# Performance work log

Hardware: AMD Instinct MI355X
Metric: run time of the kernel (lower is better)

Reference implementation:

```python
import jax, jax.numpy as jnp
import numpy as np

B, S, E, H = 4, 2048, 1024, 16
DK = E // H

def setup_inputs() -> dict:
    key = jax.random.key(0)
    ks = jax.random.split(key, 5)
    scale = 1.0 / np.sqrt(E)
    return {
        "x":  jax.random.normal(ks[0], (B, S, E), dtype=jnp.float32),
        "Wq": jax.random.normal(ks[1], (E, E), dtype=jnp.float32) * scale,
        "Wk": jax.random.normal(ks[2], (E, E), dtype=jnp.float32) * scale,
        "Wv": jax.random.normal(ks[3], (E, E), dtype=jnp.float32) * scale,
        "Wo": jax.random.normal(ks[4], (E, E), dtype=jnp.float32) * scale,
    }

def reference(x, Wq, Wk, Wv, Wo):
    b, s, e = x.shape
    # nn.Linear (no bias): y = x @ W.T
    def split_heads(t):  # (b, s, e) -> (b, H, s, DK)
        return t.reshape(b, s, H, DK).transpose(0, 2, 1, 3)
    Q = split_heads(x @ Wq.T)
    K = split_heads(x @ Wk.T)
    V = split_heads(x @ Wv.T)
    scores = jnp.einsum('bhqd,bhkd->bhqk', Q, K) / jnp.sqrt(jnp.float32(DK))
    attn = jax.nn.softmax(scores, axis=-1)  # dropout p=0.0 -> identity
    ctx = jnp.einsum('bhqk,bhkd->bhqd', attn, V)
    concat = ctx.transpose(0, 2, 1, 3).reshape(b, s, e)
    return concat @ Wo.T
```

## Files before the change

kernel.cpp:

```cpp
#include <hip/hip_runtime.h>


typedef __bf16 bf16x8 __attribute__((ext_vector_type(8)));
typedef __bf16 bf16x4 __attribute__((ext_vector_type(4)));
typedef float floatx4 __attribute__((ext_vector_type(4)));
typedef unsigned int uint2v __attribute__((ext_vector_type(2)));

#define GLOAD_LDS16(gp, lp) __builtin_amdgcn_global_load_lds( \
    (const __attribute__((address_space(1))) unsigned int*)(gp), \
    (__attribute__((address_space(3))) unsigned int*)(lp), 16, 0, 0)

__global__ __launch_bounds__(256) void cvt_x(const float4* __restrict__ s,
                                             bf16x4* __restrict__ d, int n4) {
    int i = blockIdx.x * 256 + threadIdx.x;
    if (i < n4) {
        float4 v = s[i];
        bf16x4 o = { (__bf16)v.x, (__bf16)v.y, (__bf16)v.z, (__bf16)v.w };
        d[i] = o;
    }
}

__global__ __launch_bounds__(256) void cvt_w(const float4* __restrict__ Wq,
                                             const float4* __restrict__ Wk,
                                             const float4* __restrict__ Wv,
                                             const float4* __restrict__ Wo,
                                             bf16x4* __restrict__ oq, bf16x4* __restrict__ ok,
                                             bf16x4* __restrict__ ov, bf16x4* __restrict__ oo,
                                             float qscale) {
    int y = blockIdx.y;
    const float4* s = (y == 0) ? Wq : (y == 1) ? Wk : (y == 2) ? Wv : Wo;
    bf16x4* d = (y == 0) ? oq : (y == 1) ? ok : (y == 2) ? ov : oo;
    float scale = (y == 0) ? qscale : 1.0f;
    int i = blockIdx.x * 256 + threadIdx.x;
    float4 v = s[i];
    bf16x4 o = { (__bf16)(v.x * scale), (__bf16)(v.y * scale),
                 (__bf16)(v.z * scale), (__bf16)(v.w * scale) };
    d[i] = o;
}


__device__ __forceinline__ void gemm_stage(const __bf16* __restrict__ A,
                                           const __bf16* __restrict__ W,
                                           __bf16* Asm, __bf16* Bsm,
                                           int bm, int bn, int k0, int w, int lane) {
#pragma unroll
    for (int j = 0; j < 2; ++j) {
        int base = j * 256 + w * 64;
        int flat = base + lane;
        int c = flat >> 7, r = flat & 127;
        GLOAD_LDS16(A + (size_t)(bm + r) * 1024 + k0 + c * 8, (char*)Asm + base * 16);
    }
#pragma unroll
    for (int j = 0; j < 4; ++j) {
        int base = j * 256 + w * 64;
        int flat = base + lane;
        int c = flat >> 8, r = flat & 255;
        GLOAD_LDS16(W + (size_t)(bn + r) * 1024 + k0 + c * 8, (char*)Bsm + base * 16);
    }
}

__device__ __forceinline__ void gemm_phase(const __bf16* __restrict__ A,
                                           const __bf16* __restrict__ W,
                                           const __bf16* Asm_r, const __bf16* Bsm_r,
                                           __bf16* Asm_s, __bf16* Bsm_s,
                                           int bm, int bn, int ks,
                                           int w, int lane, int quad, int l15,
                                           int wy, int wx,
                                           floatx4 acc[4][8]) {
    gemm_stage(A, W, Asm_s, Bsm_s, bm, bn, ks, w, lane);
    __builtin_amdgcn_sched_barrier(0);
    asm volatile("s_waitcnt vmcnt(12)" ::: "memory");
    __builtin_amdgcn_s_barrier();
    __builtin_amdgcn_sched_barrier(0);

    bf16x8 af[4], bf[8];
#pragma unroll
    for (int mt = 0; mt < 4; ++mt)
        af[mt] = *(const bf16x8*)(Asm_r + (quad * 128 + wy * 64 + mt * 16 + l15) * 8);
#pragma unroll
    for (int nt = 0; nt < 8; ++nt)
        bf[nt] = *(const bf16x8*)(Bsm_r + (quad * 256 + wx * 128 + nt * 16 + l15) * 8);
#pragma unroll
    for (int mt = 0; mt < 4; ++mt)
#pragma unroll
        for (int nt = 0; nt < 8; ++nt)
            acc[mt][nt] = __builtin_amdgcn_mfma_f32_16x16x32_bf16(af[mt], bf[nt],
                                                                  acc[mt][nt], 0, 0, 0);
    __builtin_amdgcn_sched_barrier(0);
    __builtin_amdgcn_s_barrier();
}

__device__ __forceinline__ void gemm_mainloop3(const __bf16* __restrict__ A,
                                               const __bf16* __restrict__ W,
                                               __bf16* SM,
                                               int bm, int bn, int tid,
                                               floatx4 acc[4][8]) {
    const int w = tid >> 6, lane = tid & 63;
    const int quad = lane >> 4, l15 = lane & 15;
    const int wy = w >> 1, wx = w & 1;
    __bf16* As[3] = { SM, SM + 12288, SM + 24576 };
    __bf16* Bs[3] = { SM + 4096, SM + 16384, SM + 28672 };
#pragma unroll
    for (int i = 0; i < 4; ++i)
#pragma unroll
        for (int j = 0; j < 8; ++j) acc[i][j] = (floatx4){0.f, 0.f, 0.f, 0.f};

    gemm_stage(A, W, As[0], Bs[0], bm, bn, 0, w, lane);
    gemm_stage(A, W, As[1], Bs[1], bm, bn, 32, w, lane);

    for (int t = 0; t < 30; t += 3) {
        gemm_phase(A, W, As[0], Bs[0], As[2], Bs[2], bm, bn, (t + 2) * 32,
                   w, lane, quad, l15, wy, wx, acc);
        gemm_phase(A, W, As[1], Bs[1], As[0], Bs[0], bm, bn, (t + 3) * 32,
                   w, lane, quad, l15, wy, wx, acc);
        gemm_phase(A, W, As[2], Bs[2], As[1], Bs[1], bm, bn, (t + 4) * 32,
                   w, lane, quad, l15, wy, wx, acc);
    }
    gemm_phase(A, W, As[0], Bs[0], As[2], Bs[2], bm, bn, 1024,
               w, lane, quad, l15, wy, wx, acc);
    gemm_phase(A, W, As[1], Bs[1], As[0], Bs[0], bm, bn, 1056,
               w, lane, quad, l15, wy, wx, acc);
    __syncthreads();
}

__global__ __launch_bounds__(256, 2) void gemm_qkv(const __bf16* __restrict__ A,
                                                   const __bf16* __restrict__ Wqb,
                                                   const __bf16* __restrict__ Wkb,
                                                   const __bf16* __restrict__ Wvb,
                                                   __bf16* __restrict__ Qg,
                                                   __bf16* __restrict__ Kg,
                                                   __bf16* __restrict__ Vtg) {
    __shared__ alignas(16) __bf16 SM[36864];
    const int sel = blockIdx.x >> 2;
    const __bf16* W = (sel == 0) ? Wqb : (sel == 1) ? Wkb : Wvb;
    __bf16* ob = (sel == 0) ? Qg : (sel == 1) ? Kg : Vtg;
    const int bm = blockIdx.y * 128, bn = (blockIdx.x & 3) * 256;
    const int tid = threadIdx.x;
    const int w = tid >> 6, lane = tid & 63;
    const int quad = lane >> 4, l15 = lane & 15;
    const int wy = w >> 1, wx = w & 1;

    floatx4 acc[4][8];
    gemm_mainloop3(A, W, SM, bm, bn, tid, acc);

    float* tb = (float*)SM + w * 272;
    const int rr = lane >> 2, c0 = (lane & 3) * 4;
#pragma unroll
    for (int mt = 0; mt < 4; ++mt)
#pragma unroll
        for (int nt = 0; nt < 8; ++nt) {
            if (sel == 2) {
#pragma unroll
                for (int r = 0; r < 4; ++r) tb[l15 * 17 + quad * 4 + r] = acc[mt][nt][r];
            } else {
#pragma unroll
                for (int r = 0; r < 4; ++r) tb[(quad * 4 + r) * 17 + l15] = acc[mt][nt][r];
            }
            float f0 = tb[rr * 17 + c0 + 0], f1 = tb[rr * 17 + c0 + 1];
            float f2 = tb[rr * 17 + c0 + 2], f3 = tb[rr * 17 + c0 + 3];
            bf16x4 pk = { (__bf16)f0, (__bf16)f1, (__bf16)f2, (__bf16)f3 };
            if (sel <= 1) {
                int m = bm + wy * 64 + mt * 16 + rr;
                int n0 = bn + wx * 128 + nt * 16 + c0;
                int bI = m >> 11, s = m & 2047, h = n0 >> 6, d0 = n0 & 63;
                *(bf16x4*)(ob + ((size_t)(bI * 16 + h) * 2048 + s) * 64 + d0) = pk;
            } else {
                int m0 = bm + wy * 64 + mt * 16 + c0;
                int n = bn + wx * 128 + nt * 16 + rr;
                int bI = m0 >> 11, s0 = m0 & 2047, h = n >> 6, d = n & 63;
                *(bf16x4*)(ob + ((size_t)(bI * 16 + h) * 64 + d) * 2048 + s0) = pk;
            }
        }
}

__global__ __launch_bounds__(256, 2) void gemm_out(const __bf16* __restrict__ A,
                                                   const __bf16* __restrict__ W,
                                                   float* __restrict__ of) {
    __shared__ alignas(16) __bf16 SM[36864];
    const int tid = threadIdx.x;
    const int lane = tid & 63, w = tid >> 6;
    const int quad = lane >> 4, l15 = lane & 15;
    const int wy = w >> 1, wx = w & 1;
    const int bm = blockIdx.y * 128, bn = blockIdx.x * 256;

    floatx4 acc[4][8];
    gemm_mainloop3(A, W, SM, bm, bn, tid, acc);

#pragma unroll
    for (int mt = 0; mt < 4; ++mt)
#pragma unroll
        for (int nt = 0; nt < 8; ++nt)
#pragma unroll
            for (int r = 0; r < 4; ++r) {
                int m = bm + wy * 64 + mt * 16 + quad * 4 + r;
                int n = bn + wx * 128 + nt * 16 + l15;
                of[(size_t)m * 1024 + n] = acc[mt][nt][r];
            }
}


__device__ __forceinline__ int paddr(int c, int row) {
    int r2 = row ^ (((row >> 3) & 1) << 1) ^ (c & 1);
    return (c * 32 + r2) * 16;
}

__device__ __forceinline__ void attn_stage(const __bf16* __restrict__ Kg,
                                           const __bf16* __restrict__ Vtg,
                                           __bf16* Ks, __bf16* Vs,
                                           int bh, int kv0, int w, int lane) {
#pragma unroll
    for (int j = 0; j < 2; ++j) {
        int base = j * 256 + w * 64;
        int flat = base + lane;
        int c = flat >> 6, r = flat & 63;
        GLOAD_LDS16(Kg + ((size_t)bh * 2048 + kv0 + r) * 64 + c * 8, (char*)Ks + base * 16);
        GLOAD_LDS16(Vtg + ((size_t)bh * 64 + r) * 2048 + kv0 + c * 8, (char*)Vs + base * 16);
    }
}

__device__ __forceinline__ void attn_phase(const __bf16* __restrict__ Kg,
                                           const __bf16* __restrict__ Vtg,
                                           const __bf16* Ksr, const __bf16* Vsr,
                                           __bf16* Kss, __bf16* Vss,
                                           char* Pw, const bf16x8 qf[2][2],
                                           int bh, int kv_next,
                                           int w, int lane, int quad, int l15,
                                           float l_p[2], floatx4 o[2][4]) {
    attn_stage(Kg, Vtg, Kss, Vss, bh, kv_next * 64, w, lane);
    __builtin_amdgcn_sched_barrier(0);
    asm volatile("s_waitcnt vmcnt(4)" ::: "memory");
    __builtin_amdgcn_s_barrier();
    __builtin_amdgcn_sched_barrier(0);

    floatx4 sa[2][4];
#pragma unroll
    for (int mt = 0; mt < 2; ++mt)
#pragma unroll
        for (int nt = 0; nt < 4; ++nt) sa[mt][nt] = (floatx4){0.f, 0.f, 0.f, 0.f};
#pragma unroll
    for (int nt = 0; nt < 4; ++nt) {
        bf16x8 kb0 = *(const bf16x8*)(Ksr + (quad * 64 + nt * 16 + l15) * 8);
        bf16x8 kb1 = *(const bf16x8*)(Ksr + ((4 + quad) * 64 + nt * 16 + l15) * 8);
#pragma unroll
        for (int mt = 0; mt < 2; ++mt) {
            sa[mt][nt] = __builtin_amdgcn_mfma_f32_16x16x32_bf16(kb0, qf[mt][0],
                                                                sa[mt][nt], 0, 0, 0);
            sa[mt][nt] = __builtin_amdgcn_mfma_f32_16x16x32_bf16(kb1, qf[mt][1],
                                                                sa[mt][nt], 0, 0, 0);
        }
    }

#pragma unroll
    for (int mt = 0; mt < 2; ++mt)
#pragma unroll
        for (int nt = 0; nt < 4; ++nt) {
            float p0 = __builtin_amdgcn_exp2f(sa[mt][nt][0]);
            float p1 = __builtin_amdgcn_exp2f(sa[mt][nt][1]);
            float p2 = __builtin_amdgcn_exp2f(sa[mt][nt][2]);
            float p3 = __builtin_amdgcn_exp2f(sa[mt][nt][3]);
            l_p[mt] += (p0 + p1) + (p2 + p3);
            unsigned u0 = __builtin_bit_cast(unsigned, p0);
            unsigned u1 = __builtin_bit_cast(unsigned, p1);
            unsigned u2 = __builtin_bit_cast(unsigned, p2);
            unsigned u3 = __builtin_bit_cast(unsigned, p3);
            uint2v pk;
            pk.x = __builtin_amdgcn_perm(u1, u0, 0x07060302);
            pk.y = __builtin_amdgcn_perm(u3, u2, 0x07060302);
            *(uint2v*)(Pw + paddr(nt * 2 + (quad >> 1), mt * 16 + l15)
                       + (quad & 1) * 8) = pk;
        }

#pragma unroll
    for (int kk = 0; kk < 2; ++kk) {
        bf16x8 pa0 = *(const bf16x8*)(Pw + paddr(kk * 4 + quad, l15));
        bf16x8 pa1 = *(const bf16x8*)(Pw + paddr(kk * 4 + quad, 16 + l15));
#pragma unroll
        for (int dt = 0; dt < 4; ++dt) {
            bf16x8 vb = *(const bf16x8*)(Vsr + ((kk * 4 + quad) * 64 + dt * 16 + l15) * 8);
            o[0][dt] = __builtin_amdgcn_mfma_f32_16x16x32_bf16(pa0, vb, o[0][dt], 0, 0, 0);
            o[1][dt] = __builtin_amdgcn_mfma_f32_16x16x32_bf16(pa1, vb, o[1][dt], 0, 0, 0);
        }
    }
    __builtin_amdgcn_sched_barrier(0);
    __builtin_amdgcn_s_barrier();
}

__global__ __launch_bounds__(256, 3) void attn_kernel(const __bf16* __restrict__ Qg,
                                                      const __bf16* __restrict__ Kg,
                                                      const __bf16* __restrict__ Vtg,
                                                      __bf16* __restrict__ ctxg) {
    __shared__ alignas(16) __bf16 Ksm0[4096];
    __shared__ alignas(16) __bf16 Vsm0[4096];
    __shared__ alignas(16) __bf16 Ksm1[4096];
    __shared__ alignas(16) __bf16 Vsm1[4096];
    __shared__ alignas(16) __bf16 Psm[8192];
    const int tid = threadIdx.x;
    const int w = tid >> 6, lane = tid & 63;
    const int quad = lane >> 4, l15 = lane & 15;

    const int orig = blockIdx.x;
    const int wg = (orig & 7) * 128 + (orig >> 3);
    const int qbase = (wg & 15) * 128;
    const int bh = wg >> 4;

    char* Pw = (char*)Psm + w * 4096;

    bf16x8 qf[2][2];
#pragma unroll
    for (int mt = 0; mt < 2; ++mt) {
        const __bf16* qrow = Qg + ((size_t)bh * 2048 + qbase + w * 32 + mt * 16 + l15) * 64;
        qf[mt][0] = *(const bf16x8*)(qrow + quad * 8);
        qf[mt][1] = *(const bf16x8*)(qrow + 32 + quad * 8);
    }

    float l_p[2] = {0.f, 0.f};
    floatx4 o[2][4];
#pragma unroll
    for (int mt = 0; mt < 2; ++mt)
#pragma unroll
        for (int dt = 0; dt < 4; ++dt) o[mt][dt] = (floatx4){0.f, 0.f, 0.f, 0.f};

    attn_stage(Kg, Vtg, Ksm0, Vsm0, bh, 0, w, lane);

    for (int kv = 0; kv < 32; kv += 2) {
        attn_phase(Kg, Vtg, Ksm0, Vsm0, Ksm1, Vsm1, Pw, qf, bh, kv + 1,
                   w, lane, quad, l15, l_p, o);
        attn_phase(Kg, Vtg, Ksm1, Vsm1, Ksm0, Vsm0, Pw, qf, bh, (kv + 2) & 31,
                   w, lane, quad, l15, l_p, o);
    }

    __syncthreads();

    float invr[2][4];
    {
        float inv[2];
#pragma unroll
        for (int mt = 0; mt < 2; ++mt) {
            float t = l_p[mt];
            t += __shfl_xor(t, 16);
            t += __shfl_xor(t, 32);
            inv[mt] = 1.f / t;
        }
#pragma unroll
        for (int mt = 0; mt < 2; ++mt)
#pragma unroll
            for (int r = 0; r < 4; ++r)
                invr[mt][r] = __shfl(inv[mt], quad * 4 + r);
    }

    float* tb = (float*)Ksm0 + w * 272;
    const int bI = bh >> 4, h = bh & 15;
    const int rr = lane >> 2, c0 = (lane & 3) * 4;
#pragma unroll
    for (int mt = 0; mt < 2; ++mt)
#pragma unroll
        for (int dt = 0; dt < 4; ++dt) {
#pragma unroll
            for (int r = 0; r < 4; ++r)
                tb[(quad * 4 + r) * 17 + l15] = o[mt][dt][r] * invr[mt][r];
            float f0 = tb[rr * 17 + c0 + 0], f1 = tb[rr * 17 + c0 + 1];
            float f2 = tb[rr * 17 + c0 + 2], f3 = tb[rr * 17 + c0 + 3];
            bf16x4 pk = { (__bf16)f0, (__bf16)f1, (__bf16)f2, (__bf16)f3 };
            *(bf16x4*)(ctxg + ((size_t)(bI * 2048 + qbase + w * 32 + mt * 16 + rr)) * 1024
                       + h * 64 + dt * 16 + c0) = pk;
        }
}

extern "C" void kernel_launch(void* const* d_in, const int* in_sizes, int n_in,
                              void* d_out, int out_size, void* d_ws, size_t ws_size,
                              hipStream_t stream) {
    const float* x  = (const float*)d_in[0];
    const float* Wq = (const float*)d_in[1];
    const float* Wk = (const float*)d_in[2];
    const float* Wv = (const float*)d_in[3];
    const float* Wo = (const float*)d_in[4];
    float* out = (float*)d_out;
    char* ws = (char*)d_ws;

    __bf16* xb  = (__bf16*)(ws);
    __bf16* wqb = (__bf16*)(ws + (16u << 20));
    __bf16* wkb = (__bf16*)(ws + (18u << 20));
    __bf16* wvb = (__bf16*)(ws + (20u << 20));
    __bf16* wob = (__bf16*)(ws + (22u << 20));
    __bf16* Qg  = (__bf16*)(ws + (24u << 20));
    __bf16* Kg  = (__bf16*)(ws + (40u << 20));
    __bf16* Vtg = (__bf16*)(ws + (56u << 20));
    __bf16* ctx = xb;

    const float qscale = 0.18033688011112042f;

    cvt_x<<<8192, 256, 0, stream>>>((const float4*)x, (bf16x4*)xb, 2097152);
    cvt_w<<<dim3(1024, 4), 256, 0, stream>>>((const float4*)Wq, (const float4*)Wk,
                                             (const float4*)Wv, (const float4*)Wo,
                                             (bf16x4*)wqb, (bf16x4*)wkb,
                                             (bf16x4*)wvb, (bf16x4*)wob, qscale);

    gemm_qkv<<<dim3(12, 64), 256, 0, stream>>>(xb, wqb, wkb, wvb, Qg, Kg, Vtg);

    attn_kernel<<<1024, 256, 0, stream>>>(Qg, Kg, Vtg, ctx);

    gemm_out<<<dim3(4, 64), 256, 0, stream>>>(ctx, wob, out);
}
```

Measured before the change: 322.3 us.

## Use double-buffered GEMM and single-buffered V in attention to raise occupancy

The GEMM mainloop drops from triple to double buffering, which shrinks shared memory so launch bounds can go from 2 to 3 blocks per CU, with the vmcnt wait adjusted to match. The attention kernel now keeps one V buffer loaded in the same phase it is consumed, adds an extra barrier and wait before the PV product, and drops the swizzled P layout in favour of a plain one read as two 8-byte halves. Occupancy rises to 4 blocks, at the cost of less prefetch distance for V and possible LDS bank conflicts on P. The last phase now prefetches K tile 32, which lies past the end of the sequence.

```diff
diff --git a/kernel.cpp b/kernel.cpp
--- a/kernel.cpp
+++ b/kernel.cpp
@@ -69,7 +69,7 @@
                                            floatx4 acc[4][8]) {
     gemm_stage(A, W, Asm_s, Bsm_s, bm, bn, ks, w, lane);
     __builtin_amdgcn_sched_barrier(0);
-    asm volatile("s_waitcnt vmcnt(12)" ::: "memory");
+    asm volatile("s_waitcnt vmcnt(6)" ::: "memory");
     __builtin_amdgcn_s_barrier();
     __builtin_amdgcn_sched_barrier(0);
 
@@ -90,7 +90,7 @@
     __builtin_amdgcn_s_barrier();
 }
 
-__device__ __forceinline__ void gemm_mainloop3(const __bf16* __restrict__ A,
+__device__ __forceinline__ void gemm_mainloop2(const __bf16* __restrict__ A,
                                                const __bf16* __restrict__ W,
                                                __bf16* SM,
                                                int bm, int bn, int tid,
@@ -98,39 +98,34 @@
     const int w = tid >> 6, lane = tid & 63;
     const int quad = lane >> 4, l15 = lane & 15;
     const int wy = w >> 1, wx = w & 1;
-    __bf16* As[3] = { SM, SM + 12288, SM + 24576 };
-    __bf16* Bs[3] = { SM + 4096, SM + 16384, SM + 28672 };
+    __bf16* Asm0 = SM;
+    __bf16* Bsm0 = SM + 4096;
+    __bf16* Asm1 = SM + 12288;
+    __bf16* Bsm1 = SM + 16384;
 #pragma unroll
     for (int i = 0; i < 4; ++i)
 #pragma unroll
         for (int j = 0; j < 8; ++j) acc[i][j] = (floatx4){0.f, 0.f, 0.f, 0.f};
 
-    gemm_stage(A, W, As[0], Bs[0], bm, bn, 0, w, lane);
-    gemm_stage(A, W, As[1], Bs[1], bm, bn, 32, w, lane);
-
-    for (int t = 0; t < 30; t += 3) {
-        gemm_phase(A, W, As[0], Bs[0], As[2], Bs[2], bm, bn, (t + 2) * 32,
+    gemm_stage(A, W, Asm0, Bsm0, bm, bn, 0, w, lane);
+
+    for (int k0 = 0; k0 < 1024; k0 += 64) {
+        gemm_phase(A, W, Asm0, Bsm0, Asm1, Bsm1, bm, bn, k0 + 32,
                    w, lane, quad, l15, wy, wx, acc);
-        gemm_phase(A, W, As[1], Bs[1], As[0], Bs[0], bm, bn, (t + 3) * 32,
+        gemm_phase(A, W, Asm1, Bsm1, Asm0, Bsm0, bm, bn, k0 + 64,
                    w, lane, quad, l15, wy, wx, acc);
-        gemm_phase(A, W, As[2], Bs[2], As[1], Bs[1], bm, bn, (t + 4) * 32,
-                   w, lane, quad, l15, wy, wx, acc);
-    }
-    gemm_phase(A, W, As[0], Bs[0], As[2], Bs[2], bm, bn, 1024,
-               w, lane, quad, l15, wy, wx, acc);
-    gemm_phase(A, W, As[1], Bs[1], As[0], Bs[0], bm, bn, 1056,
-               w, lane, quad, l15, wy, wx, acc);
+    }
     __syncthreads();
 }
 
-__global__ __launch_bounds__(256, 2) void gemm_qkv(const __bf16* __restrict__ A,
+__global__ __launch_bounds__(256, 3) void gemm_qkv(const __bf16* __restrict__ A,
                                                    const __bf16* __restrict__ Wqb,
                                                    const __bf16* __restrict__ Wkb,
                                                    const __bf16* __restrict__ Wvb,
                                                    __bf16* __restrict__ Qg,
                                                    __bf16* __restrict__ Kg,
                                                    __bf16* __restrict__ Vtg) {
-    __shared__ alignas(16) __bf16 SM[36864];
+    __shared__ alignas(16) __bf16 SM[24576];
     const int sel = blockIdx.x >> 2;
     const __bf16* W = (sel == 0) ? Wqb : (sel == 1) ? Wkb : Wvb;
     __bf16* ob = (sel == 0) ? Qg : (sel == 1) ? Kg : Vtg;
@@ -141,7 +136,7 @@
     const int wy = w >> 1, wx = w & 1;
 
     floatx4 acc[4][8];
-    gemm_mainloop3(A, W, SM, bm, bn, tid, acc);
+    gemm_mainloop2(A, W, SM, bm, bn, tid, acc);
 
     float* tb = (float*)SM + w * 272;
     const int rr = lane >> 2, c0 = (lane & 3) * 4;
@@ -173,10 +168,10 @@
         }
 }
 
-__global__ __launch_bounds__(256, 2) void gemm_out(const __bf16* __restrict__ A,
+__global__ __launch_bounds__(256, 3) void gemm_out(const __bf16* __restrict__ A,
                                                    const __bf16* __restrict__ W,
                                                    float* __restrict__ of) {
-    __shared__ alignas(16) __bf16 SM[36864];
+    __shared__ alignas(16) __bf16 SM[24576];
     const int tid = threadIdx.x;
     const int lane = tid & 63, w = tid >> 6;
     const int quad = lane >> 4, l15 = lane & 15;
@@ -184,7 +179,7 @@
     const int bm = blockIdx.y * 128, bn = blockIdx.x * 256;
 
     floatx4 acc[4][8];
-    gemm_mainloop3(A, W, SM, bm, bn, tid, acc);
+    gemm_mainloop2(A, W, SM, bm, bn, tid, acc);
 
 #pragma unroll
     for (int mt = 0; mt < 4; ++mt)
@@ -199,34 +194,42 @@
 }
 
 
-__device__ __forceinline__ int paddr(int c, int row) {
-    int r2 = row ^ (((row >> 3) & 1) << 1) ^ (c & 1);
-    return (c * 32 + r2) * 16;
-}
-
-__device__ __forceinline__ void attn_stage(const __bf16* __restrict__ Kg,
-                                           const __bf16* __restrict__ Vtg,
-                                           __bf16* Ks, __bf16* Vs,
-                                           int bh, int kv0, int w, int lane) {
+__device__ __forceinline__ void attn_stage_K(const __bf16* __restrict__ Kg,
+                                             __bf16* Ks, int bh, int kv0,
+                                             int w, int lane) {
 #pragma unroll
     for (int j = 0; j < 2; ++j) {
         int base = j * 256 + w * 64;
         int flat = base + lane;
         int c = flat >> 6, r = flat & 63;
         GLOAD_LDS16(Kg + ((size_t)bh * 2048 + kv0 + r) * 64 + c * 8, (char*)Ks + base * 16);
+    }
+}
+
+__device__ __forceinline__ void attn_stage_V(const __bf16* __restrict__ Vtg,
+                                             __bf16* Vs, int bh, int kv0,
+                                             int w, int lane) {
+#pragma unroll
+    for (int j = 0; j < 2; ++j) {
+        int base = j * 256 + w * 64;
+        int flat = base + lane;
+        int c = flat >> 6, r = flat & 63;
         GLOAD_LDS16(Vtg + ((size_t)bh * 64 + r) * 2048 + kv0 + c * 8, (char*)Vs + base * 16);
     }
 }
 
 __device__ __forceinline__ void attn_phase(const __bf16* __restrict__ Kg,
                                            const __bf16* __restrict__ Vtg,
-                                           const __bf16* Ksr, const __bf16* Vsr,
-                                           __bf16* Kss, __bf16* Vss,
+                                           const __bf16* Ksr, __bf16* Kss,
+                                           __bf16* Vsm,
                                            char* Pw, const bf16x8 qf[2][2],
-                                           int bh, int kv_next,
+                                           int bh, int kv_cur, int kv_next,
                                            int w, int lane, int quad, int l15,
                                            float l_p[2], floatx4 o[2][4]) {
-    attn_stage(Kg, Vtg, Kss, Vss, bh, kv_next * 64, w, lane);
+    __builtin_amdgcn_s_barrier();
+    __builtin_amdgcn_sched_barrier(0);
+    attn_stage_V(Vtg, Vsm, bh, kv_cur * 64, w, lane);
+    attn_stage_K(Kg, Kss, bh, kv_next * 64, w, lane);
     __builtin_amdgcn_sched_barrier(0);
     asm volatile("s_waitcnt vmcnt(4)" ::: "memory");
     __builtin_amdgcn_s_barrier();
@@ -266,33 +269,40 @@
             uint2v pk;
             pk.x = __builtin_amdgcn_perm(u1, u0, 0x07060302);
             pk.y = __builtin_amdgcn_perm(u3, u2, 0x07060302);
-            *(uint2v*)(Pw + paddr(nt * 2 + (quad >> 1), mt * 16 + l15)
-                       + (quad & 1) * 8) = pk;
-        }
+            *(uint2v*)(Pw + ((nt * 4 + quad) * 32 + mt * 16 + l15) * 8) = pk;
+        }
+
+    __builtin_amdgcn_sched_barrier(0);
+    asm volatile("s_waitcnt vmcnt(2)" ::: "memory");
+    __builtin_amdgcn_s_barrier();
+    __builtin_amdgcn_sched_barrier(0);
 
 #pragma unroll
     for (int kk = 0; kk < 2; ++kk) {
-        bf16x8 pa0 = *(const bf16x8*)(Pw + paddr(kk * 4 + quad, l15));
-        bf16x8 pa1 = *(const bf16x8*)(Pw + paddr(kk * 4 + quad, 16 + l15));
+        const int c4a = (kk * 4 + quad) * 2;
+        bf16x4 lo0 = *(const bf16x4*)(Pw + (c4a * 32 + l15) * 8);
+        bf16x4 hi0 = *(const bf16x4*)(Pw + ((c4a + 1) * 32 + l15) * 8);
+        bf16x4 lo1 = *(const bf16x4*)(Pw + (c4a * 32 + 16 + l15) * 8);
+        bf16x4 hi1 = *(const bf16x4*)(Pw + ((c4a + 1) * 32 + 16 + l15) * 8);
+        bf16x8 pa0 = __builtin_shufflevector(lo0, hi0, 0, 1, 2, 3, 4, 5, 6, 7);
+        bf16x8 pa1 = __builtin_shufflevector(lo1, hi1, 0, 1, 2, 3, 4, 5, 6, 7);
 #pragma unroll
         for (int dt = 0; dt < 4; ++dt) {
-            bf16x8 vb = *(const bf16x8*)(Vsr + ((kk * 4 + quad) * 64 + dt * 16 + l15) * 8);
+            bf16x8 vb = *(const bf16x8*)(Vsm + ((kk * 4 + quad) * 64 + dt * 16 + l15) * 8);
             o[0][dt] = __builtin_amdgcn_mfma_f32_16x16x32_bf16(pa0, vb, o[0][dt], 0, 0, 0);
             o[1][dt] = __builtin_amdgcn_mfma_f32_16x16x32_bf16(pa1, vb, o[1][dt], 0, 0, 0);
         }
     }
     __builtin_amdgcn_sched_barrier(0);
-    __builtin_amdgcn_s_barrier();
-}
-
-__global__ __launch_bounds__(256, 3) void attn_kernel(const __bf16* __restrict__ Qg,
+}
+
+__global__ __launch_bounds__(256, 4) void attn_kernel(const __bf16* __restrict__ Qg,
                                                       const __bf16* __restrict__ Kg,
                                                       const __bf16* __restrict__ Vtg,
                                                       __bf16* __restrict__ ctxg) {
     __shared__ alignas(16) __bf16 Ksm0[4096];
-    __shared__ alignas(16) __bf16 Vsm0[4096];
     __shared__ alignas(16) __bf16 Ksm1[4096];
-    __shared__ alignas(16) __bf16 Vsm1[4096];
+    __shared__ alignas(16) __bf16 Vsm[4096];
     __shared__ alignas(16) __bf16 Psm[8192];
     const int tid = threadIdx.x;
     const int w = tid >> 6, lane = tid & 63;
@@ -320,12 +330,12 @@
 #pragma unroll
         for (int dt = 0; dt < 4; ++dt) o[mt][dt] = (floatx4){0.f, 0.f, 0.f, 0.f};
 
-    attn_stage(Kg, Vtg, Ksm0, Vsm0, bh, 0, w, lane);
+    attn_stage_K(Kg, Ksm0, bh, 0, w, lane);
 
     for (int kv = 0; kv < 32; kv += 2) {
-        attn_phase(Kg, Vtg, Ksm0, Vsm0, Ksm1, Vsm1, Pw, qf, bh, kv + 1,
+        attn_phase(Kg, Vtg, Ksm0, Ksm1, Vsm, Pw, qf, bh, kv, kv + 1,
                    w, lane, quad, l15, l_p, o);
-        attn_phase(Kg, Vtg, Ksm1, Vsm1, Ksm0, Vsm0, Pw, qf, bh, (kv + 2) & 31,
+        attn_phase(Kg, Vtg, Ksm1, Ksm0, Vsm, Pw, qf, bh, kv + 1, kv + 2,
                    w, lane, quad, l15, l_p, o);
     }
 
```

After: 514.9 us. +59.7%, slower.
